# Kernel optimization log

Hardware: AMD Instinct MI355X
Metric: run time of the kernel (lower is better)

## Reference

```python
import jax, jax.numpy as jnp
import numpy as np

N = 50000
E = 800000
D_IN = 64
D_E = 32
H = 128
EPS = 1e-5


def _seg_mean(msgs, dst, n):
    s = jax.ops.segment_sum(msgs, dst, num_segments=n)
    c = jax.ops.segment_sum(jnp.ones((dst.shape[0], 1), msgs.dtype), dst, num_segments=n)
    return s / jnp.maximum(c, 1.0)


def _bn(h, g, b, m, v):
    return g * (h - m) * jax.lax.rsqrt(v + EPS) + b


def setup_inputs() -> dict:
    key = jax.random.key(0)
    ks = jax.random.split(key, 32)
    inp = {
        "x": jax.random.normal(ks[0], (N, D_IN), jnp.float32),
        "edge_index_0": jax.random.randint(ks[1], (2, E), 0, N),
        "edge_index_1": jax.random.randint(ks[2], (2, E), 0, N),
        "edge_index_2": jax.random.randint(ks[3], (2, E), 0, N),
        "edge_attr_0": jax.random.normal(ks[4], (E, D_E), jnp.float32),
        # conv1: Linear(D_IN + D_E -> H)
        "W1": jax.random.normal(ks[5], (H, D_IN + D_E), jnp.float32) * 0.1,
        "b1": jnp.zeros((H,), jnp.float32),
        "g1": jnp.ones((H,), jnp.float32), "be1": jnp.zeros((H,), jnp.float32),
        "m1": jax.random.normal(ks[6], (H,), jnp.float32) * 0.1,
        "v1": jax.random.uniform(ks[7], (H,), jnp.float32) + 0.5,
        # SAGEConv2: lin_l (bias) on aggregated neighbors + lin_r (no bias) on self
        "Wl2": jax.random.normal(ks[8], (H, H), jnp.float32) * 0.1,
        "bl2": jnp.zeros((H,), jnp.float32),
        "Wr2": jax.random.normal(ks[9], (H, H), jnp.float32) * 0.1,
        "g2": jnp.ones((H,), jnp.float32), "be2": jnp.zeros((H,), jnp.float32),
        "m2": jax.random.normal(ks[10], (H,), jnp.float32) * 0.1,
        "v2": jax.random.uniform(ks[11], (H,), jnp.float32) + 0.5,
        # SAGEConv3
        "Wl3": jax.random.normal(ks[12], (H, H), jnp.float32) * 0.1,
        "bl3": jnp.zeros((H,), jnp.float32),
        "Wr3": jax.random.normal(ks[13], (H, H), jnp.float32) * 0.1,
        "g3": jnp.ones((H,), jnp.float32), "be3": jnp.zeros((H,), jnp.float32),
        "m3": jax.random.normal(ks[14], (H,), jnp.float32) * 0.1,
        "v3": jax.random.uniform(ks[15], (H,), jnp.float32) + 0.5,
        # mlp: Linear(H + D_IN -> 64) -> ReLU -> Linear(64 -> 1)
        "W4": jax.random.normal(ks[16], (64, H + D_IN), jnp.float32) * 0.1,
        "b4": jnp.zeros((64,), jnp.float32),
        "W5": jax.random.normal(ks[17], (1, 64), jnp.float32) * 0.1,
        "b5": jnp.zeros((1,), jnp.float32),
    }
    return inp


def reference(x, edge_index_0, edge_index_1, edge_index_2, edge_attr_0,
              W1, b1, g1, be1, m1, v1,
              Wl2, bl2, Wr2, g2, be2, m2, v2,
              Wl3, bl3, Wr3, g3, be3, m3, v3,
              W4, b4, W5, b5):
    n = x.shape[0]
    init = x
    # conv1: gather x_j + edge_attr, concat, linear, mean scatter, relu (update)
    msg = jnp.concatenate([x[edge_index_0[0]], edge_attr_0], axis=-1) @ W1.T + b1  # [E,H]
    h = jax.nn.relu(_seg_mean(msg, edge_index_0[1], n))
    h = jax.nn.relu(_bn(h, g1, be1, m1, v1))  # dropout: eval (identity)
    # conv2: SAGEConv = lin_l(mean_j x_j) + lin_r(x)
    agg = _seg_mean(h[edge_index_1[0]], edge_index_1[1], n)
    h = agg @ Wl2.T + bl2 + h @ Wr2.T
    h = jax.nn.relu(_bn(h, g2, be2, m2, v2))
    # conv3
    agg = _seg_mean(h[edge_index_2[0]], edge_index_2[1], n)
    h = agg @ Wl3.T + bl3 + h @ Wr3.T
    h = jax.nn.relu(_bn(h, g3, be3, m3, v3))
    # readout mlp on [h, initial_embedding]
    z = jnp.concatenate([h, init], axis=1)
    z = jax.nn.relu(z @ W4.T + b4)
    out = (z @ W5.T + b5).squeeze(-1)  # [N]
    return out
```

## Files before the change

### kernel.cpp

```cpp
#include <hip/hip_runtime.h>
#include <hip/hip_bf16.h>
#include <stdint.h>

#define NN 50000
#define NE 800000
#define EPS 1e-5f

#define KB 196
#define SH 8
#define NPB 256
#define RCAP 4500
#define PT2 2048
#define NT2 391

typedef __attribute__((ext_vector_type(8))) short bf16x8;
typedef __attribute__((ext_vector_type(4))) float floatx4;

static __device__ __forceinline__ float bf2f(unsigned int u){
  union { unsigned int i; float f; } c; c.i = u << 16; return c.f;
}
static __device__ __forceinline__ unsigned short f2bf(float f){
  union { float f; unsigned int i; } c; c.f = f;
  unsigned int x = c.i;
  return (unsigned short)((x + 0x7fffu + ((x >> 16) & 1u)) >> 16);
}

#define CVT_X   3200000
#define CVT_W1  3212288
#define CVT_WL2 3228672
#define CVT_WR2 3245056
#define CVT_WL3 3261440
#define CVT_WR3 3277824
#define CVT_END 3290112
__global__ void k_cvt_all(const float* __restrict__ x,  const float* __restrict__ W1,
                          const float* __restrict__ Wl2, const float* __restrict__ Wr2,
                          const float* __restrict__ Wl3, const float* __restrict__ Wr3,
                          const float* __restrict__ W4,
                          unsigned short* __restrict__ xb,  unsigned short* __restrict__ W1b,
                          unsigned short* __restrict__ Wl2b, unsigned short* __restrict__ Wr2b,
                          unsigned short* __restrict__ Wl3b, unsigned short* __restrict__ Wr3b,
                          unsigned short* __restrict__ W4b, int* __restrict__ gcur){
  int i = blockIdx.x * 256 + threadIdx.x;
  if(i >= CVT_END) return;
  if(i < 3 * KB) gcur[i] = 0;
  if(i < CVT_X)        xb[i] = f2bf(x[i]);
  else if(i < CVT_W1)  W1b[i - CVT_X]    = f2bf(W1[i - CVT_X]);
  else if(i < CVT_WL2) Wl2b[i - CVT_W1]  = f2bf(Wl2[i - CVT_W1]);
  else if(i < CVT_WR2) Wr2b[i - CVT_WL2] = f2bf(Wr2[i - CVT_WL2]);
  else if(i < CVT_WL3) Wl3b[i - CVT_WR2] = f2bf(Wl3[i - CVT_WR2]);
  else if(i < CVT_WR3) Wr3b[i - CVT_WL3] = f2bf(Wr3[i - CVT_WL3]);
  else                 W4b[i - CVT_WR3]  = f2bf(W4[i - CVT_WR3]);
}

__global__ void k_part3(const int* __restrict__ ei0, const int* __restrict__ ei1,
                        const int* __restrict__ ei2, int* __restrict__ gcur,
                        int2* __restrict__ rec, int* __restrict__ recE){
  __shared__ int2 stage[PT2];
  __shared__ int stE[PT2];
  __shared__ int hist[KB], ex[KB], cur[KB], gbase[KB];
  __shared__ int part[256];
  __shared__ int tot;
  int layer = blockIdx.x % 3;
  int tile = (blockIdx.x / 3) * PT2;
  const int* ei = (layer == 0) ? ei0 : ((layer == 1) ? ei1 : ei2);
  int2* recL = rec + (size_t)layer * KB * RCAP;
  int* gcurL = gcur + layer * KB;
  int tid = threadIdx.x;
  for(int i = tid; i < KB; i += 256) hist[i] = 0;
  __syncthreads();
  int dst[8], src[8];
  #pragma unroll
  for(int j = 0; j < 8; j++){
    int e = tile + j * 256 + tid;
    if(e < NE){ src[j] = ei[e]; dst[j] = ei[NE + e]; atomicAdd(&hist[dst[j] >> SH], 1); }
    else dst[j] = -1;
  }
  __syncthreads();
  int c0 = (tid < KB) ? hist[tid] : 0;
  part[tid] = c0;
  __syncthreads();
  for(int d = 1; d < 256; d <<= 1){
    int v = (tid >= d) ? part[tid - d] : 0;
    __syncthreads();
    part[tid] += v;
    __syncthreads();
  }
  if(tid < KB){
    int e = part[tid] - c0;
    ex[tid] = e; cur[tid] = e;
    gbase[tid] = atomicAdd(&gcurL[tid], c0);
  }
  if(tid == 255) tot = part[255];
  __syncthreads();
  #pragma unroll
  for(int j = 0; j < 8; j++){
    if(dst[j] >= 0){
      int b = dst[j] >> SH;
      int s = atomicAdd(&cur[b], 1);
      stage[s] = make_int2(dst[j], src[j]);
      if(layer == 0) stE[s] = tile + j * 256 + tid;
    }
  }
  __syncthreads();
  for(int s = tid; s < tot; s += 256){
    int2 r = stage[s];
    int b = r.x >> SH;
    int idx = b * RCAP + gbase[b] + (s - ex[b]);
    recL[idx] = r;
    if(layer == 0) recE[idx] = stE[s];
  }
}

__global__ void k_build3(const int2* __restrict__ rec, const int* __restrict__ recE,
                         const int* __restrict__ gcnt,
                         int2* __restrict__ adj2, int* __restrict__ adjI1, int* __restrict__ adjI2,
                         int* __restrict__ rowbeg3, int* __restrict__ deg3){
  __shared__ int cnt[NPB], cur2[NPB];
  __shared__ int part[256];
  int layer = blockIdx.x % 3;
  int b = blockIdx.x / 3;
  int tid = threadIdx.x;
  int n0 = b << SH;
  int nr = gcnt[layer * KB + b];
  const int2* r = rec + ((size_t)layer * KB + b) * RCAP;
  const int* re = recE + (size_t)b * RCAP;
  cnt[tid] = 0;
  __syncthreads();
  for(int k = tid; k < nr; k += 256) atomicAdd(&cnt[r[k].x - n0], 1);
  __syncthreads();
  int c0 = cnt[tid];
  part[tid] = c0;
  __syncthreads();
  for(int d = 1; d < 256; d <<= 1){
    int v = (tid >= d) ? part[tid - d] : 0;
    __syncthreads();
    part[tid] += v;
    __syncthreads();
  }
  int base = part[tid] - c0;
  cur2[tid] = base;
  __syncthreads();
  int n = n0 + tid;
  if(n < NN){ rowbeg3[layer * NN + n] = b * RCAP + base; deg3[layer * NN + n] = c0; }
  for(int k = tid; k < nr; k += 256){
    int2 q = r[k];
    int p = atomicAdd(&cur2[q.x - n0], 1);
    if(layer == 0)      adj2[b * RCAP + p]  = make_int2(q.y, re[k]);
    else if(layer == 1) adjI1[b * RCAP + p] = q.y;
    else                adjI2[b * RCAP + p] = q.y;
  }
}

__global__ void k_aggXE(const int* __restrict__ rowbeg, const int* __restrict__ deg,
                        const int2* __restrict__ adj2,
                        const unsigned short* __restrict__ xb, const float* __restrict__ ea,
                        unsigned short* __restrict__ agg){
  int w = (blockIdx.x * blockDim.x + threadIdx.x) >> 6;
  int lane = threadIdx.x & 63;
  if(w >= NN) return;
  int sub = lane >> 4, li = lane & 15;
  int r0 = rowbeg[w], dg = deg[w], r1 = r0 + dg;
  float acc[8] = {0.f,0.f,0.f,0.f,0.f,0.f,0.f,0.f};
  for(int k = r0; k < r1; k += 8){
    int e0 = k + sub, e1 = k + 4 + sub;
    int i0 = e0 < r1 ? e0 : r1 - 1;
    int i1 = e1 < r1 ? e1 : r1 - 1;
    float m0 = e0 < r1 ? 1.f : 0.f;
    float m1 = e1 < r1 ? 1.f : 0.f;
    int2 a0 = adj2[i0], a1 = adj2[i1];
    if(li < 8){
      uint4 v0 = *(const uint4*)(xb + (size_t)a0.x * 64 + li * 8);
      uint4 v1 = *(const uint4*)(xb + (size_t)a1.x * 64 + li * 8);
      acc[0] += m0 * bf2f(v0.x & 0xffffu); acc[1] += m0 * bf2f(v0.x >> 16);
      acc[2] += m0 * bf2f(v0.y & 0xffffu); acc[3] += m0 * bf2f(v0.y >> 16);
      acc[4] += m0 * bf2f(v0.z & 0xffffu); acc[5] += m0 * bf2f(v0.z >> 16);
      acc[6] += m0 * bf2f(v0.w & 0xffffu); acc[7] += m0 * bf2f(v0.w >> 16);
      acc[0] += m1 * bf2f(v1.x & 0xffffu); acc[1] += m1 * bf2f(v1.x >> 16);
      acc[2] += m1 * bf2f(v1.y & 0xffffu); acc[3] += m1 * bf2f(v1.y >> 16);
      acc[4] += m1 * bf2f(v1.z & 0xffffu); acc[5] += m1 * bf2f(v1.z >> 16);
      acc[6] += m1 * bf2f(v1.w & 0xffffu); acc[7] += m1 * bf2f(v1.w >> 16);
    } else {
      int j = li - 8;
      float4 p0 = *(const float4*)(ea + (size_t)a0.y * 32 + j * 4);
      float4 p1 = *(const float4*)(ea + (size_t)a1.y * 32 + j * 4);
      acc[0] += m0 * p0.x; acc[1] += m0 * p0.y;
      acc[2] += m0 * p0.z; acc[3] += m0 * p0.w;
      acc[0] += m1 * p1.x; acc[1] += m1 * p1.y;
      acc[2] += m1 * p1.z; acc[3] += m1 * p1.w;
    }
  }
  #pragma unroll
  for(int d = 16; d < 64; d <<= 1){
    #pragma unroll
    for(int i = 0; i < 8; i++) acc[i] += __shfl_xor(acc[i], d, 64);
  }
  if(sub == 0){
    float inv = 1.0f / (float)(dg > 0 ? dg : 1);
    if(li < 8){
      unsigned int q0 = (unsigned int)f2bf(acc[0]*inv) | ((unsigned int)f2bf(acc[1]*inv) << 16);
      unsigned int q1 = (unsigned int)f2bf(acc[2]*inv) | ((unsigned int)f2bf(acc[3]*inv) << 16);
      unsigned int q2 = (unsigned int)f2bf(acc[4]*inv) | ((unsigned int)f2bf(acc[5]*inv) << 16);
      unsigned int q3 = (unsigned int)f2bf(acc[6]*inv) | ((unsigned int)f2bf(acc[7]*inv) << 16);
      *(uint4*)(agg + (size_t)w * 96 + li * 8) = make_uint4(q0, q1, q2, q3);
    } else {
      int j = li - 8;
      unsigned int q0 = (unsigned int)f2bf(acc[0]*inv) | ((unsigned int)f2bf(acc[1]*inv) << 16);
      unsigned int q1 = (unsigned int)f2bf(acc[2]*inv) | ((unsigned int)f2bf(acc[3]*inv) << 16);
      *(uint2*)(agg + (size_t)w * 96 + 64 + j * 4) = make_uint2(q0, q1);
    }
  }
}

__global__ void k_aggH(const int* __restrict__ rowbeg, const int* __restrict__ deg,
                       const int* __restrict__ adj,
                       const unsigned short* __restrict__ h, unsigned short* __restrict__ agg){
  int w = (blockIdx.x * blockDim.x + threadIdx.x) >> 6;
  int lane = threadIdx.x & 63;
  if(w >= NN) return;
  int sub = lane >> 4, li = lane & 15;
  int r0 = rowbeg[w], dg = deg[w], r1 = r0 + dg;
  float acc[8] = {0.f,0.f,0.f,0.f,0.f,0.f,0.f,0.f};
  for(int k = r0; k < r1; k += 8){
    int e0 = k + sub, e1 = k + 4 + sub;
    int i0 = e0 < r1 ? e0 : r1 - 1;
    int i1 = e1 < r1 ? e1 : r1 - 1;
    float m0 = e0 < r1 ? 1.f : 0.f;
    float m1 = e1 < r1 ? 1.f : 0.f;
    int s0 = adj[i0], s1 = adj[i1];
    uint4 v0 = *(const uint4*)(h + (size_t)s0 * 128 + li * 8);
    uint4 v1 = *(const uint4*)(h + (size_t)s1 * 128 + li * 8);
    acc[0] += m0 * bf2f(v0.x & 0xffffu); acc[1] += m0 * bf2f(v0.x >> 16);
    acc[2] += m0 * bf2f(v0.y & 0xffffu); acc[3] += m0 * bf2f(v0.y >> 16);
    acc[4] += m0 * bf2f(v0.z & 0xffffu); acc[5] += m0 * bf2f(v0.z >> 16);
    acc[6] += m0 * bf2f(v0.w & 0xffffu); acc[7] += m0 * bf2f(v0.w >> 16);
    acc[0] += m1 * bf2f(v1.x & 0xffffu); acc[1] += m1 * bf2f(v1.x >> 16);
    acc[2] += m1 * bf2f(v1.y & 0xffffu); acc[3] += m1 * bf2f(v1.y >> 16);
    acc[4] += m1 * bf2f(v1.z & 0xffffu); acc[5] += m1 * bf2f(v1.z >> 16);
    acc[6] += m1 * bf2f(v1.w & 0xffffu); acc[7] += m1 * bf2f(v1.w >> 16);
  }
  #pragma unroll
  for(int d = 16; d < 64; d <<= 1){
    #pragma unroll
    for(int i = 0; i < 8; i++) acc[i] += __shfl_xor(acc[i], d, 64);
  }
  if(sub == 0){
    float inv = 1.0f / (float)(dg > 0 ? dg : 1);
    unsigned int p0 = (unsigned int)f2bf(acc[0]*inv) | ((unsigned int)f2bf(acc[1]*inv) << 16);
    unsigned int p1 = (unsigned int)f2bf(acc[2]*inv) | ((unsigned int)f2bf(acc[3]*inv) << 16);
    unsigned int p2 = (unsigned int)f2bf(acc[4]*inv) | ((unsigned int)f2bf(acc[5]*inv) << 16);
    unsigned int p3 = (unsigned int)f2bf(acc[6]*inv) | ((unsigned int)f2bf(acc[7]*inv) << 16);
    *(uint4*)(agg + (size_t)w * 128 + li * 8) = make_uint4(p0, p1, p2, p3);
  }
}

__global__ void k_lin1(const unsigned short* __restrict__ agg, const unsigned short* __restrict__ W1,
                       const float* __restrict__ b1,
                       const float* __restrict__ g1, const float* __restrict__ be1,
                       const float* __restrict__ m1, const float* __restrict__ v1,
                       const int* __restrict__ deg, unsigned short* __restrict__ h1){
  int wave = (blockIdx.x * blockDim.x + threadIdx.x) >> 6;
  int lane = threadIdx.x & 63;
  int mt = wave >> 3, nt = wave & 7;
  if(mt >= 3125) return;
  int node0 = mt * 16;
  int col = lane & 15, quad = lane >> 4;
  int o = nt * 16 + col;
  int arow = node0 + col;
  floatx4 acc = {0.f, 0.f, 0.f, 0.f};
  #pragma unroll
  for(int kc = 0; kc < 3; kc++){
    bf16x8 a = *(const bf16x8*)(agg + arow * 96 + kc * 32 + quad * 8);
    bf16x8 b = *(const bf16x8*)(W1 + o * 96 + kc * 32 + quad * 8);
    acc = __builtin_amdgcn_mfma_f32_16x16x32_bf16(a, b, acc, 0, 0, 0);
  }
  float bb = b1[o];
  float sc = g1[o] * rsqrtf(v1[o] + EPS);
  float mv = m1[o], bev = be1[o];
  #pragma unroll
  for(int r = 0; r < 4; r++){
    int node = node0 + quad * 4 + r;
    float pre = (deg[node] > 0) ? (acc[r] + bb) : 0.0f;
    float t = fmaxf(pre, 0.f);
    float bn = sc * (t - mv) + bev;
    h1[node * 128 + o] = f2bf(fmaxf(bn, 0.f));
  }
}

__global__ void k_sage(const unsigned short* __restrict__ agg, const unsigned short* __restrict__ hin,
                       const unsigned short* __restrict__ Wl, const float* __restrict__ bl,
                       const unsigned short* __restrict__ Wr,
                       const float* __restrict__ g, const float* __restrict__ be,
                       const float* __restrict__ m, const float* __restrict__ v,
                       unsigned short* __restrict__ hout){
  int wave = (blockIdx.x * blockDim.x + threadIdx.x) >> 6;
  int lane = threadIdx.x & 63;
  int mt = wave >> 3, nt = wave & 7;
  if(mt >= 3125) return;
  int node0 = mt * 16;
  int col = lane & 15, quad = lane >> 4;
  int o = nt * 16 + col;
  int arow = node0 + col;
  floatx4 acc = {0.f, 0.f, 0.f, 0.f};
  #pragma unroll
  for(int kc = 0; kc < 4; kc++){
    bf16x8 a = *(const bf16x8*)(agg + arow * 128 + kc * 32 + quad * 8);
    bf16x8 b = *(const bf16x8*)(Wl + o * 128 + kc * 32 + quad * 8);
    acc = __builtin_amdgcn_mfma_f32_16x16x32_bf16(a, b, acc, 0, 0, 0);
  }
  #pragma unroll
  for(int kc = 0; kc < 4; kc++){
    bf16x8 a = *(const bf16x8*)(hin + arow * 128 + kc * 32 + quad * 8);
    bf16x8 b = *(const bf16x8*)(Wr + o * 128 + kc * 32 + quad * 8);
    acc = __builtin_amdgcn_mfma_f32_16x16x32_bf16(a, b, acc, 0, 0, 0);
  }
  float blv = bl[o];
  float sc = g[o] * rsqrtf(v[o] + EPS);
  float mv = m[o], bev = be[o];
  #pragma unroll
  for(int r = 0; r < 4; r++){
    int node = node0 + quad * 4 + r;
    float pre = acc[r] + blv;
    float bn = sc * (pre - mv) + bev;
    hout[node * 128 + o] = f2bf(fmaxf(bn, 0.f));
  }
}

__global__ void k_readout(const unsigned short* __restrict__ h3, const unsigned short* __restrict__ xb,
                          const unsigned short* __restrict__ W4, const float* __restrict__ b4,
                          const float* __restrict__ W5, const float* __restrict__ b5,
                          float* __restrict__ out){
  int wave = (blockIdx.x * blockDim.x + threadIdx.x) >> 6;
  int lane = threadIdx.x & 63;
  if(wave >= 3125) return;
  int node0 = wave * 16;
  int col = lane & 15, quad = lane >> 4;
  int arow = node0 + col;
  float partial[4] = {0.f, 0.f, 0.f, 0.f};
  #pragma unroll
  for(int nt = 0; nt < 4; nt++){
    int o = nt * 16 + col;
    floatx4 acc = {0.f, 0.f, 0.f, 0.f};
    #pragma unroll
    for(int kc = 0; kc < 4; kc++){
      bf16x8 a = *(const bf16x8*)(h3 + arow * 128 + kc * 32 + quad * 8);
      bf16x8 b = *(const bf16x8*)(W4 + o * 192 + kc * 32 + quad * 8);
      acc = __builtin_amdgcn_mfma_f32_16x16x32_bf16(a, b, acc, 0, 0, 0);
    }
    #pragma unroll
    for(int kc = 0; kc < 2; kc++){
      bf16x8 a = *(const bf16x8*)(xb + arow * 64 + kc * 32 + quad * 8);
      bf16x8 b = *(const bf16x8*)(W4 + o * 192 + 128 + kc * 32 + quad * 8);
      acc = __builtin_amdgcn_mfma_f32_16x16x32_bf16(a, b, acc, 0, 0, 0);
    }
    float bb = b4[o];
    float w5 = W5[o];
    #pragma unroll
    for(int r = 0; r < 4; r++)
      partial[r] += fmaxf(acc[r] + bb, 0.f) * w5;
  }
  #pragma unroll
  for(int d = 1; d < 16; d <<= 1){
    #pragma unroll
    for(int r = 0; r < 4; r++)
      partial[r] += __shfl_xor(partial[r], d, 64);
  }
  if(col == 0){
    float b5f = b5[0];
    #pragma unroll
    for(int r = 0; r < 4; r++)
      out[node0 + quad * 4 + r] = partial[r] + b5f;
  }
}

extern "C" void kernel_launch(void* const* d_in, const int* in_sizes, int n_in,
                              void* d_out, int out_size, void* d_ws, size_t ws_size,
                              hipStream_t stream) {
  const float* x   = (const float*)d_in[0];
  const int* ei0   = (const int*)d_in[1];
  const int* ei1   = (const int*)d_in[2];
  const int* ei2   = (const int*)d_in[3];
  const float* ea  = (const float*)d_in[4];
  const float* W1  = (const float*)d_in[5];
  const float* b1  = (const float*)d_in[6];
  const float* g1  = (const float*)d_in[7];
  const float* be1 = (const float*)d_in[8];
  const float* m1  = (const float*)d_in[9];
  const float* v1  = (const float*)d_in[10];
  const float* Wl2 = (const float*)d_in[11];
  const float* bl2 = (const float*)d_in[12];
  const float* Wr2 = (const float*)d_in[13];
  const float* g2  = (const float*)d_in[14];
  const float* be2 = (const float*)d_in[15];
  const float* m2  = (const float*)d_in[16];
  const float* v2  = (const float*)d_in[17];
  const float* Wl3 = (const float*)d_in[18];
  const float* bl3 = (const float*)d_in[19];
  const float* Wr3 = (const float*)d_in[20];
  const float* g3  = (const float*)d_in[21];
  const float* be3 = (const float*)d_in[22];
  const float* m3  = (const float*)d_in[23];
  const float* v3  = (const float*)d_in[24];
  const float* W4  = (const float*)d_in[25];
  const float* b4  = (const float*)d_in[26];
  const float* W5  = (const float*)d_in[27];
  const float* b5  = (const float*)d_in[28];

  char* ws = (char*)d_ws;
  size_t off = 0;
  auto alloc = [&](size_t bytes) -> void* {
    void* p = (void*)(ws + off);
    off += (bytes + 255) & ~(size_t)255;
    return p;
  };
  int* gcur    = (int*)alloc(3 * KB * sizeof(int));
  int* rowbeg3 = (int*)alloc(3 * NN * sizeof(int));
  int* deg3    = (int*)alloc(3 * NN * sizeof(int));
  char* uni    = (char*)alloc((size_t)3 * NN * 128 * 2);
  int2* adj2   = (int2*)alloc((size_t)KB * RCAP * 8);
  int* adjI1   = (int*)alloc((size_t)KB * RCAP * 4);
  int* adjI2   = (int*)alloc((size_t)KB * RCAP * 4);
  unsigned short* agg1 = (unsigned short*)alloc((size_t)NN * 96 * 2);
  unsigned short* xb   = (unsigned short*)alloc((size_t)NN * 64 * 2);
  unsigned short* W1b  = (unsigned short*)alloc(12288 * 2);
  unsigned short* Wl2b = (unsigned short*)alloc(16384 * 2);
  unsigned short* Wr2b = (unsigned short*)alloc(16384 * 2);
  unsigned short* Wl3b = (unsigned short*)alloc(16384 * 2);
  unsigned short* Wr3b = (unsigned short*)alloc(16384 * 2);
  unsigned short* W4b  = (unsigned short*)alloc(12288 * 2);

  int2* recDS = (int2*)uni;
  int* recE   = (int*)(uni + (((size_t)3 * KB * RCAP * 8 + 255) & ~(size_t)255));
  unsigned short* h1   = (unsigned short*)uni;
  unsigned short* aggH = h1 + (size_t)NN * 128;
  unsigned short* h2   = h1 + (size_t)2 * NN * 128;
  unsigned short* h3   = h1;

  int* rb0 = rowbeg3;            int* dg0 = deg3;
  int* rb1 = rowbeg3 + NN;       int* dg1 = deg3 + NN;
  int* rb2 = rowbeg3 + 2 * NN;   int* dg2 = deg3 + 2 * NN;

  const int gP3   = 3 * NT2;
  const int gB3   = 3 * KB;
  const int gAgg  = (NN * 64) / 256;
  const int gTile = (3125 * 8 * 64) / 256;
  const int gRead = (3125 * 64 + 255) / 256;
  const int gCvt  = (CVT_END + 255) / 256;

  k_cvt_all<<<gCvt, 256, 0, stream>>>(x, W1, Wl2, Wr2, Wl3, Wr3, W4,
                                      xb, W1b, Wl2b, Wr2b, Wl3b, Wr3b, W4b, gcur);

  k_part3<<<gP3, 256, 0, stream>>>(ei0, ei1, ei2, gcur, recDS, recE);
  k_build3<<<gB3, 256, 0, stream>>>(recDS, recE, gcur, adj2, adjI1, adjI2, rowbeg3, deg3);

  k_aggXE<<<gAgg, 256, 0, stream>>>(rb0, dg0, adj2, xb, ea, agg1);
  k_lin1<<<gTile, 256, 0, stream>>>(agg1, W1b, b1, g1, be1, m1, v1, dg0, h1);

  k_aggH<<<gAgg, 256, 0, stream>>>(rb1, dg1, adjI1, h1, aggH);
  k_sage<<<gTile, 256, 0, stream>>>(aggH, h1, Wl2b, bl2, Wr2b, g2, be2, m2, v2, h2);

  k_aggH<<<gAgg, 256, 0, stream>>>(rb2, dg2, adjI2, h2, aggH);
  k_sage<<<gTile, 256, 0, stream>>>(aggH, h2, Wl3b, bl3, Wr3b, g3, be3, m3, v3, h3);

  k_readout<<<gRead, 256, 0, stream>>>(h3, xb, W4b, b4, W5, b5, (float*)d_out);

  (void)in_sizes; (void)n_in; (void)out_size; (void)ws_size;
}
```

Before: 491.3 us.

## Store edge ids in partition records and pre-convert edge attributes to bf16

The partition kernel now writes only the edge id per record instead of (dst, src) pairs plus a separate edge-id array. The build kernel re-reads dst and src from the edge index through that id. In the layer-0 blocks the partition kernel also converts edge_attr to bf16 in edge order. The aggregation kernel then gathers half as many bytes of edge attributes per edge. The cost is indirect global reads of the edge index in the build kernel, plus a separate streaming conversion pass over 800K×32 floats.

Measured after the change: 579.3 us. 17.9% more time.

```diff
diff --git a/kernel.cpp b/kernel.cpp
--- a/kernel.cpp
+++ b/kernel.cpp
@@ -54,25 +54,26 @@
 
 __global__ void k_part3(const int* __restrict__ ei0, const int* __restrict__ ei1,
                         const int* __restrict__ ei2, int* __restrict__ gcur,
-                        int2* __restrict__ rec, int* __restrict__ recE){
+                        int* __restrict__ rec,
+                        const float* __restrict__ ea, unsigned int* __restrict__ eab){
   __shared__ int2 stage[PT2];
-  __shared__ int stE[PT2];
   __shared__ int hist[KB], ex[KB], cur[KB], gbase[KB];
   __shared__ int part[256];
   __shared__ int tot;
   int layer = blockIdx.x % 3;
   int tile = (blockIdx.x / 3) * PT2;
   const int* ei = (layer == 0) ? ei0 : ((layer == 1) ? ei1 : ei2);
-  int2* recL = rec + (size_t)layer * KB * RCAP;
+  int* recL = rec + (size_t)layer * KB * RCAP;
   int* gcurL = gcur + layer * KB;
   int tid = threadIdx.x;
+  int cnt_local = NE - tile; if(cnt_local > PT2) cnt_local = PT2;
   for(int i = tid; i < KB; i += 256) hist[i] = 0;
   __syncthreads();
-  int dst[8], src[8];
+  int dst[8];
   #pragma unroll
   for(int j = 0; j < 8; j++){
     int e = tile + j * 256 + tid;
-    if(e < NE){ src[j] = ei[e]; dst[j] = ei[NE + e]; atomicAdd(&hist[dst[j] >> SH], 1); }
+    if(e < NE){ dst[j] = ei[NE + e]; atomicAdd(&hist[dst[j] >> SH], 1); }
     else dst[j] = -1;
   }
   __syncthreads();
@@ -97,22 +98,28 @@
     if(dst[j] >= 0){
       int b = dst[j] >> SH;
       int s = atomicAdd(&cur[b], 1);
-      stage[s] = make_int2(dst[j], src[j]);
-      if(layer == 0) stE[s] = tile + j * 256 + tid;
+      stage[s] = make_int2(dst[j], tile + j * 256 + tid);
     }
   }
   __syncthreads();
   for(int s = tid; s < tot; s += 256){
     int2 r = stage[s];
     int b = r.x >> SH;
-    int idx = b * RCAP + gbase[b] + (s - ex[b]);
-    recL[idx] = r;
-    if(layer == 0) recE[idx] = stE[s];
-  }
-}
-
-__global__ void k_build3(const int2* __restrict__ rec, const int* __restrict__ recE,
-                         const int* __restrict__ gcnt,
+    recL[b * RCAP + gbase[b] + (s - ex[b])] = r.y;
+  }
+  if(layer == 0){
+    int g = tid >> 4, li = tid & 15;
+    for(int t = g; t < cnt_local; t += 16){
+      size_t e = (size_t)(tile + t);
+      float2 v = *(const float2*)(ea + e * 32 + li * 2);
+      eab[e * 16 + li] = (unsigned int)f2bf(v.x) | ((unsigned int)f2bf(v.y) << 16);
+    }
+  }
+}
+
+__global__ void k_build3(const int* __restrict__ rec, const int* __restrict__ gcnt,
+                         const int* __restrict__ ei0, const int* __restrict__ ei1,
+                         const int* __restrict__ ei2,
                          int2* __restrict__ adj2, int* __restrict__ adjI1, int* __restrict__ adjI2,
                          int* __restrict__ rowbeg3, int* __restrict__ deg3){
   __shared__ int cnt[NPB], cur2[NPB];
@@ -122,11 +129,14 @@
   int tid = threadIdx.x;
   int n0 = b << SH;
   int nr = gcnt[layer * KB + b];
-  const int2* r = rec + ((size_t)layer * KB + b) * RCAP;
-  const int* re = recE + (size_t)b * RCAP;
+  const int* ei = (layer == 0) ? ei0 : ((layer == 1) ? ei1 : ei2);
+  const int* r = rec + ((size_t)layer * KB + b) * RCAP;
   cnt[tid] = 0;
   __syncthreads();
-  for(int k = tid; k < nr; k += 256) atomicAdd(&cnt[r[k].x - n0], 1);
+  for(int k = tid; k < nr; k += 256){
+    int dst = ei[NE + r[k]];
+    atomicAdd(&cnt[dst - n0], 1);
+  }
   __syncthreads();
   int c0 = cnt[tid];
   part[tid] = c0;
@@ -143,17 +153,19 @@
   int n = n0 + tid;
   if(n < NN){ rowbeg3[layer * NN + n] = b * RCAP + base; deg3[layer * NN + n] = c0; }
   for(int k = tid; k < nr; k += 256){
-    int2 q = r[k];
-    int p = atomicAdd(&cur2[q.x - n0], 1);
-    if(layer == 0)      adj2[b * RCAP + p]  = make_int2(q.y, re[k]);
-    else if(layer == 1) adjI1[b * RCAP + p] = q.y;
-    else                adjI2[b * RCAP + p] = q.y;
+    int eid = r[k];
+    int dst = ei[NE + eid];
+    int src = ei[eid];
+    int p = atomicAdd(&cur2[dst - n0], 1);
+    if(layer == 0)      adj2[b * RCAP + p]  = make_int2(src, eid);
+    else if(layer == 1) adjI1[b * RCAP + p] = src;
+    else                adjI2[b * RCAP + p] = src;
   }
 }
 
 __global__ void k_aggXE(const int* __restrict__ rowbeg, const int* __restrict__ deg,
                         const int2* __restrict__ adj2,
-                        const unsigned short* __restrict__ xb, const float* __restrict__ ea,
+                        const unsigned short* __restrict__ xb, const unsigned int* __restrict__ eab,
                         unsigned short* __restrict__ agg){
   int w = (blockIdx.x * blockDim.x + threadIdx.x) >> 6;
   int lane = threadIdx.x & 63;
@@ -181,12 +193,12 @@
       acc[6] += m1 * bf2f(v1.w & 0xffffu); acc[7] += m1 * bf2f(v1.w >> 16);
     } else {
       int j = li - 8;
-      float4 p0 = *(const float4*)(ea + (size_t)a0.y * 32 + j * 4);
-      float4 p1 = *(const float4*)(ea + (size_t)a1.y * 32 + j * 4);
-      acc[0] += m0 * p0.x; acc[1] += m0 * p0.y;
-      acc[2] += m0 * p0.z; acc[3] += m0 * p0.w;
-      acc[0] += m1 * p1.x; acc[1] += m1 * p1.y;
-      acc[2] += m1 * p1.z; acc[3] += m1 * p1.w;
+      uint2 p0 = *(const uint2*)(eab + (size_t)a0.y * 16 + j * 2);
+      uint2 p1 = *(const uint2*)(eab + (size_t)a1.y * 16 + j * 2);
+      acc[0] += m0 * bf2f(p0.x & 0xffffu); acc[1] += m0 * bf2f(p0.x >> 16);
+      acc[2] += m0 * bf2f(p0.y & 0xffffu); acc[3] += m0 * bf2f(p0.y >> 16);
+      acc[0] += m1 * bf2f(p1.x & 0xffffu); acc[1] += m1 * bf2f(p1.x >> 16);
+      acc[2] += m1 * bf2f(p1.y & 0xffffu); acc[3] += m1 * bf2f(p1.y >> 16);
     }
   }
   #pragma unroll
@@ -415,7 +427,8 @@
   int* gcur    = (int*)alloc(3 * KB * sizeof(int));
   int* rowbeg3 = (int*)alloc(3 * NN * sizeof(int));
   int* deg3    = (int*)alloc(3 * NN * sizeof(int));
-  char* uni    = (char*)alloc((size_t)3 * NN * 128 * 2);
+  const size_t REC_PAD = (((size_t)3 * KB * RCAP * 4) + 255) & ~(size_t)255;
+  char* uni    = (char*)alloc(REC_PAD + (size_t)NE * 64);
   int2* adj2   = (int2*)alloc((size_t)KB * RCAP * 8);
   int* adjI1   = (int*)alloc((size_t)KB * RCAP * 4);
   int* adjI2   = (int*)alloc((size_t)KB * RCAP * 4);
@@ -428,8 +441,8 @@
   unsigned short* Wr3b = (unsigned short*)alloc(16384 * 2);
   unsigned short* W4b  = (unsigned short*)alloc(12288 * 2);
 
-  int2* recDS = (int2*)uni;
-  int* recE   = (int*)(uni + (((size_t)3 * KB * RCAP * 8 + 255) & ~(size_t)255));
+  int* recDS = (int*)uni;
+  unsigned int* eab = (unsigned int*)(uni + REC_PAD);
   unsigned short* h1   = (unsigned short*)uni;
   unsigned short* aggH = h1 + (size_t)NN * 128;
   unsigned short* h2   = h1 + (size_t)2 * NN * 128;
@@ -449,10 +462,11 @@
   k_cvt_all<<<gCvt, 256, 0, stream>>>(x, W1, Wl2, Wr2, Wl3, Wr3, W4,
                                       xb, W1b, Wl2b, Wr2b, Wl3b, Wr3b, W4b, gcur);
 
-  k_part3<<<gP3, 256, 0, stream>>>(ei0, ei1, ei2, gcur, recDS, recE);
-  k_build3<<<gB3, 256, 0, stream>>>(recDS, recE, gcur, adj2, adjI1, adjI2, rowbeg3, deg3);
-
-  k_aggXE<<<gAgg, 256, 0, stream>>>(rb0, dg0, adj2, xb, ea, agg1);
+  k_part3<<<gP3, 256, 0, stream>>>(ei0, ei1, ei2, gcur, recDS, ea, eab);
+  k_build3<<<gB3, 256, 0, stream>>>(recDS, gcur, ei0, ei1, ei2,
+                                    adj2, adjI1, adjI2, rowbeg3, deg3);
+
+  k_aggXE<<<gAgg, 256, 0, stream>>>(rb0, dg0, adj2, xb, eab, agg1);
   k_lin1<<<gTile, 256, 0, stream>>>(agg1, W1b, b1, g1, be1, m1, v1, dg0, h1);
 
   k_aggH<<<gAgg, 256, 0, stream>>>(rb1, dg1, adjI1, h1, aggH);
```

## Fuse bf16 conversion into partition kernel and drop separate edge-id record buffer

Applied to the files above, without the earlier changes.

Merges the standalone fp32-to-bf16 conversion kernel into the edge partition kernel as extra blocks and zeroes the bucket counters with an async memset instead. For layer 0 the partition record now carries the edge id in place of the source node, so the separate recE buffer and its staging are removed. The build kernel then looks up the source node via ei0[edge id], trading a random gather for less partition write traffic and one fewer launch.

Result: no change. 498.4 us (+1.4%).

```diff
diff --git a/kernel.cpp b/kernel.cpp
--- a/kernel.cpp
+++ b/kernel.cpp
@@ -12,6 +12,8 @@
 #define RCAP 4500
 #define PT2 2048
 #define NT2 391
+#define GP3 (3 * NT2)
+#define GCVT ((3290112 + 255) / 256)
 
 typedef __attribute__((ext_vector_type(8))) short bf16x8;
 typedef __attribute__((ext_vector_type(4))) float floatx4;
@@ -32,47 +34,53 @@
 #define CVT_WL3 3261440
 #define CVT_WR3 3277824
 #define CVT_END 3290112
-__global__ void k_cvt_all(const float* __restrict__ x,  const float* __restrict__ W1,
-                          const float* __restrict__ Wl2, const float* __restrict__ Wr2,
-                          const float* __restrict__ Wl3, const float* __restrict__ Wr3,
-                          const float* __restrict__ W4,
-                          unsigned short* __restrict__ xb,  unsigned short* __restrict__ W1b,
-                          unsigned short* __restrict__ Wl2b, unsigned short* __restrict__ Wr2b,
-                          unsigned short* __restrict__ Wl3b, unsigned short* __restrict__ Wr3b,
-                          unsigned short* __restrict__ W4b, int* __restrict__ gcur){
-  int i = blockIdx.x * 256 + threadIdx.x;
-  if(i >= CVT_END) return;
-  if(i < 3 * KB) gcur[i] = 0;
-  if(i < CVT_X)        xb[i] = f2bf(x[i]);
-  else if(i < CVT_W1)  W1b[i - CVT_X]    = f2bf(W1[i - CVT_X]);
-  else if(i < CVT_WL2) Wl2b[i - CVT_W1]  = f2bf(Wl2[i - CVT_W1]);
-  else if(i < CVT_WR2) Wr2b[i - CVT_WL2] = f2bf(Wr2[i - CVT_WL2]);
-  else if(i < CVT_WL3) Wl3b[i - CVT_WR2] = f2bf(Wl3[i - CVT_WR2]);
-  else if(i < CVT_WR3) Wr3b[i - CVT_WL3] = f2bf(Wr3[i - CVT_WL3]);
-  else                 W4b[i - CVT_WR3]  = f2bf(W4[i - CVT_WR3]);
-}
-
-__global__ void k_part3(const int* __restrict__ ei0, const int* __restrict__ ei1,
-                        const int* __restrict__ ei2, int* __restrict__ gcur,
-                        int2* __restrict__ rec, int* __restrict__ recE){
+
+__global__ void k_part3cvt(const int* __restrict__ ei0, const int* __restrict__ ei1,
+                           const int* __restrict__ ei2, int* __restrict__ gcur,
+                           int2* __restrict__ rec,
+                           const float* __restrict__ x,  const float* __restrict__ W1,
+                           const float* __restrict__ Wl2, const float* __restrict__ Wr2,
+                           const float* __restrict__ Wl3, const float* __restrict__ Wr3,
+                           const float* __restrict__ W4,
+                           unsigned short* __restrict__ xb,  unsigned short* __restrict__ W1b,
+                           unsigned short* __restrict__ Wl2b, unsigned short* __restrict__ Wr2b,
+                           unsigned short* __restrict__ Wl3b, unsigned short* __restrict__ Wr3b,
+                           unsigned short* __restrict__ W4b){
   __shared__ int2 stage[PT2];
-  __shared__ int stE[PT2];
   __shared__ int hist[KB], ex[KB], cur[KB], gbase[KB];
   __shared__ int part[256];
   __shared__ int tot;
+  int tid = threadIdx.x;
+
+  if(blockIdx.x >= GP3){
+    int i = (blockIdx.x - GP3) * 256 + tid;
+    if(i >= CVT_END) return;
+    if(i < CVT_X)        xb[i] = f2bf(x[i]);
+    else if(i < CVT_W1)  W1b[i - CVT_X]    = f2bf(W1[i - CVT_X]);
+    else if(i < CVT_WL2) Wl2b[i - CVT_W1]  = f2bf(Wl2[i - CVT_W1]);
+    else if(i < CVT_WR2) Wr2b[i - CVT_WL2] = f2bf(Wr2[i - CVT_WL2]);
+    else if(i < CVT_WL3) Wl3b[i - CVT_WR2] = f2bf(Wl3[i - CVT_WR2]);
+    else if(i < CVT_WR3) Wr3b[i - CVT_WL3] = f2bf(Wr3[i - CVT_WL3]);
+    else                 W4b[i - CVT_WR3]  = f2bf(W4[i - CVT_WR3]);
+    return;
+  }
+
   int layer = blockIdx.x % 3;
   int tile = (blockIdx.x / 3) * PT2;
   const int* ei = (layer == 0) ? ei0 : ((layer == 1) ? ei1 : ei2);
   int2* recL = rec + (size_t)layer * KB * RCAP;
   int* gcurL = gcur + layer * KB;
-  int tid = threadIdx.x;
   for(int i = tid; i < KB; i += 256) hist[i] = 0;
   __syncthreads();
-  int dst[8], src[8];
+  int dst[8], pay[8];
   #pragma unroll
   for(int j = 0; j < 8; j++){
     int e = tile + j * 256 + tid;
-    if(e < NE){ src[j] = ei[e]; dst[j] = ei[NE + e]; atomicAdd(&hist[dst[j] >> SH], 1); }
+    if(e < NE){
+      dst[j] = ei[NE + e];
+      pay[j] = (layer == 0) ? e : ei[e];
+      atomicAdd(&hist[dst[j] >> SH], 1);
+    }
     else dst[j] = -1;
   }
   __syncthreads();
@@ -97,22 +105,19 @@
     if(dst[j] >= 0){
       int b = dst[j] >> SH;
       int s = atomicAdd(&cur[b], 1);
-      stage[s] = make_int2(dst[j], src[j]);
-      if(layer == 0) stE[s] = tile + j * 256 + tid;
+      stage[s] = make_int2(dst[j], pay[j]);
     }
   }
   __syncthreads();
   for(int s = tid; s < tot; s += 256){
     int2 r = stage[s];
     int b = r.x >> SH;
-    int idx = b * RCAP + gbase[b] + (s - ex[b]);
-    recL[idx] = r;
-    if(layer == 0) recE[idx] = stE[s];
-  }
-}
-
-__global__ void k_build3(const int2* __restrict__ rec, const int* __restrict__ recE,
-                         const int* __restrict__ gcnt,
+    recL[b * RCAP + gbase[b] + (s - ex[b])] = r;
+  }
+}
+
+__global__ void k_build3(const int2* __restrict__ rec, const int* __restrict__ gcnt,
+                         const int* __restrict__ ei0,
                          int2* __restrict__ adj2, int* __restrict__ adjI1, int* __restrict__ adjI2,
                          int* __restrict__ rowbeg3, int* __restrict__ deg3){
   __shared__ int cnt[NPB], cur2[NPB];
@@ -123,7 +128,6 @@
   int n0 = b << SH;
   int nr = gcnt[layer * KB + b];
   const int2* r = rec + ((size_t)layer * KB + b) * RCAP;
-  const int* re = recE + (size_t)b * RCAP;
   cnt[tid] = 0;
   __syncthreads();
   for(int k = tid; k < nr; k += 256) atomicAdd(&cnt[r[k].x - n0], 1);
@@ -145,7 +149,7 @@
   for(int k = tid; k < nr; k += 256){
     int2 q = r[k];
     int p = atomicAdd(&cur2[q.x - n0], 1);
-    if(layer == 0)      adj2[b * RCAP + p]  = make_int2(q.y, re[k]);
+    if(layer == 0)      adj2[b * RCAP + p]  = make_int2(ei0[q.y], q.y);
     else if(layer == 1) adjI1[b * RCAP + p] = q.y;
     else                adjI2[b * RCAP + p] = q.y;
   }
@@ -429,7 +433,6 @@
   unsigned short* W4b  = (unsigned short*)alloc(12288 * 2);
 
   int2* recDS = (int2*)uni;
-  int* recE   = (int*)(uni + (((size_t)3 * KB * RCAP * 8 + 255) & ~(size_t)255));
   unsigned short* h1   = (unsigned short*)uni;
   unsigned short* aggH = h1 + (size_t)NN * 128;
   unsigned short* h2   = h1 + (size_t)2 * NN * 128;
@@ -439,18 +442,17 @@
   int* rb1 = rowbeg3 + NN;       int* dg1 = deg3 + NN;
   int* rb2 = rowbeg3 + 2 * NN;   int* dg2 = deg3 + 2 * NN;
 
-  const int gP3   = 3 * NT2;
   const int gB3   = 3 * KB;
   const int gAgg  = (NN * 64) / 256;
   const int gTile = (3125 * 8 * 64) / 256;
   const int gRead = (3125 * 64 + 255) / 256;
-  const int gCvt  = (CVT_END + 255) / 256;
-
-  k_cvt_all<<<gCvt, 256, 0, stream>>>(x, W1, Wl2, Wr2, Wl3, Wr3, W4,
-                                      xb, W1b, Wl2b, Wr2b, Wl3b, Wr3b, W4b, gcur);
-
-  k_part3<<<gP3, 256, 0, stream>>>(ei0, ei1, ei2, gcur, recDS, recE);
-  k_build3<<<gB3, 256, 0, stream>>>(recDS, recE, gcur, adj2, adjI1, adjI2, rowbeg3, deg3);
+
+  hipMemsetAsync(gcur, 0, 3 * KB * sizeof(int), stream);
+
+  k_part3cvt<<<GP3 + GCVT, 256, 0, stream>>>(ei0, ei1, ei2, gcur, recDS,
+                                             x, W1, Wl2, Wr2, Wl3, Wr3, W4,
+                                             xb, W1b, Wl2b, Wr2b, Wl3b, Wr3b, W4b);
+  k_build3<<<gB3, 256, 0, stream>>>(recDS, gcur, ei0, adj2, adjI1, adjI2, rowbeg3, deg3);
 
   k_aggXE<<<gAgg, 256, 0, stream>>>(rb0, dg0, adj2, xb, ea, agg1);
   k_lin1<<<gTile, 256, 0, stream>>>(agg1, W1b, b1, g1, be1, m1, v1, dg0, h1);
```
